# Kernel optimization log

Hardware: AMD Instinct MI355X
Metric: run time of the kernel (lower is better)

The kernel has to match this reference:

```python
import jax, jax.numpy as jnp
import numpy as np

N = 50000      # nodes
E = 1600000    # edges (avg degree 32)
IN, H, OUT, ED = 16, 128, 64, 16


def setup_inputs() -> dict:
    key = jax.random.key(0)
    ks = jax.random.split(key, 24)

    def w(k, shape):
        return jax.random.normal(k, shape, jnp.float32) / np.float32(np.sqrt(shape[0]))

    inp = {
        "x": jax.random.normal(ks[0], (N, IN), jnp.float32),
        "edge_attr": jax.random.normal(ks[1], (E, ED), jnp.float32),
        "edge_src": jax.random.randint(ks[2], (E,), 0, N, jnp.int32),
        "edge_dst": jax.random.randint(ks[3], (E,), 0, N, jnp.int32),
    }
    dims = [(IN, H, H), (H, H, H), (H, H, OUT)]
    i = 4
    for l, (din, dh, dout) in enumerate(dims):
        inp[f"we{l}"] = w(ks[i], (ED, din)); inp[f"be{l}"] = jnp.zeros((din,), jnp.float32)
        inp[f"w1{l}"] = w(ks[i + 1], (din, dh)); inp[f"b1{l}"] = jnp.zeros((dh,), jnp.float32)
        inp[f"w2{l}"] = w(ks[i + 2], (dh, dout)); inp[f"b2{l}"] = jnp.zeros((dout,), jnp.float32)
        i += 3
    inp["rw1"] = w(ks[i], (OUT, H)); inp["rb1"] = jnp.zeros((H,), jnp.float32)
    inp["rw2"] = w(ks[i + 1], (H, IN)); inp["rb2"] = jnp.zeros((IN,), jnp.float32)
    return inp


def reference(x, edge_attr, edge_src, edge_dst,
              we0, be0, w10, b10, w20, b20,
              we1, be1, w11, b11, w21, b21,
              we2, be2, w12, b12, w22, b22,
              rw1, rb1, rw2, rb2):
    layers = [(we0, be0, w10, b10, w20, b20),
              (we1, be1, w11, b11, w21, b21),
              (we2, be2, w12, b12, w22, b22)]
    n = x.shape[0]

    def phi(h):
        # GIN with edge features (GINE): h_i = MLP(h_i + sum_j relu(h_j + W_e e_ij))
        for idx, (we, be, w1, b1, w2, b2) in enumerate(layers):
            e = edge_attr @ we + be                                  # [E, d_in]
            msg = jax.nn.relu(h[edge_src] + e)                       # [E, d_in]
            agg = jax.ops.segment_sum(msg, edge_dst, num_segments=n)  # [N, d_in]
            h = jax.nn.relu((h + agg) @ w1 + b1) @ w2 + b2           # conv MLP
            if idx < len(layers) - 1:
                h = jax.nn.relu(h)
        return h

    out = phi(x) + phi(-x)                       # sign invariance, [N, OUT]
    out = jax.nn.relu(out @ rw1 + rb1) @ rw2 + rb2  # rho readout, [N, IN]
    return out
```

## Files before the change

kernel.cpp:

```cpp
#include <hip/hip_runtime.h>

constexpr int DHID = 128;

__device__ __forceinline__ float b2f(unsigned short u) {
    union { unsigned int i; float f; } v;
    v.i = ((unsigned int)u) << 16;
    return v.f;
}
__device__ __forceinline__ unsigned short f2b(float f) {
    union { float f; unsigned int i; } v;
    v.f = f;
    unsigned int x = v.i;
    return (unsigned short)((x + 0x7fff + ((x >> 16) & 1)) >> 16);
}
__device__ __forceinline__ unsigned int pack2(float a, float b) {
    return (unsigned int)f2b(a) | ((unsigned int)f2b(b) << 16);
}
__device__ __forceinline__ float bres(float w) { return w - b2f(f2b(w)); }
__device__ __forceinline__ void dot2b(float& acc, unsigned int a, unsigned int b) {
    asm("v_dot2_f32_bf16 %0, %1, %2, %0" : "+v"(acc) : "v"(a), "v"(b));
}

__global__ __launch_bounds__(256)
void init_h0(const float* __restrict__ x, float* __restrict__ H0,
             unsigned short* __restrict__ H0B, int n) {
    int i = blockIdx.x * 256 + threadIdx.x;
    if (i < n * 16) {
        int r = i >> 4, c = i & 15;
        float v = x[i];
        H0[(size_t)(2 * r) * 16 + c] = v;
        H0[(size_t)(2 * r + 1) * 16 + c] = -v;
        H0B[(size_t)(2 * r) * 16 + c] = f2b(v);
        H0B[(size_t)(2 * r + 1) * 16 + c] = f2b(-v);
    }
}

__global__ __launch_bounds__(256)
void sum_signs(const float* __restrict__ H3, float* __restrict__ S, int n) {
    int i = blockIdx.x * 256 + threadIdx.x;
    if (i < n * 64) {
        int r = i >> 6;
        S[i] = H3[i + (size_t)r * 64] + H3[i + (size_t)r * 64 + 64];
    }
}

__global__ __launch_bounds__(256)
void csr_count(const int* __restrict__ DST, int* __restrict__ deg, int E_) {
    int e = blockIdx.x * 256 + threadIdx.x;
    if (e < E_) atomicAdd(&deg[DST[e]], 1);
}

__global__ __launch_bounds__(256)
void scan1(const int* __restrict__ deg, int* __restrict__ off,
           int* __restrict__ bsum, int n) {
    __shared__ int s[256];
    int tid = threadIdx.x;
    int i = blockIdx.x * 256 + tid;
    int v = (i < n) ? deg[i] : 0;
    s[tid] = v;
    __syncthreads();
    for (int d = 1; d < 256; d <<= 1) {
        int t = (tid >= d) ? s[tid - d] : 0;
        __syncthreads();
        if (tid >= d) s[tid] += t;
        __syncthreads();
    }
    if (i < n) off[i] = s[tid] - v;
    if (tid == 255) bsum[blockIdx.x] = s[255];
}

__global__ __launch_bounds__(256)
void scan2(int* __restrict__ bsum, int nb) {
    __shared__ int s[256];
    int tid = threadIdx.x;
    int v = (tid < nb) ? bsum[tid] : 0;
    s[tid] = v;
    __syncthreads();
    for (int d = 1; d < 256; d <<= 1) {
        int t = (tid >= d) ? s[tid - d] : 0;
        __syncthreads();
        if (tid >= d) s[tid] += t;
        __syncthreads();
    }
    if (tid < nb) bsum[tid] = s[tid] - v;
}

__global__ __launch_bounds__(256)
void scan3(int* __restrict__ off, int* __restrict__ pos,
           const int* __restrict__ bsum, const int* __restrict__ deg, int n) {
    int i = blockIdx.x * 256 + threadIdx.x;
    if (i < n) {
        int o = off[i] + bsum[blockIdx.x];
        off[i] = o;
        pos[i] = o;
        if (i == n - 1) off[n] = o + deg[i];
    }
}

__global__ __launch_bounds__(256)
void csr_fill(const int* __restrict__ SRC, const int* __restrict__ DST,
              const float* __restrict__ EA, int* __restrict__ pos,
              int* __restrict__ csrsrc, uint4* __restrict__ EABS, int E_) {
    int e = blockIdx.x * 256 + threadIdx.x;
    if (e < E_) {
        int d = DST[e];
        int j = atomicAdd(&pos[d], 1);
        csrsrc[j] = SRC[e];
        const float4* ea4 = (const float4*)(EA + (size_t)e * 16);
        float4 q0 = ea4[0], q1 = ea4[1], q2 = ea4[2], q3 = ea4[3];
        uint4 o0, o1;
        o0.x = pack2(q0.x, q0.y); o0.y = pack2(q0.z, q0.w);
        o0.z = pack2(q1.x, q1.y); o0.w = pack2(q1.z, q1.w);
        o1.x = pack2(q2.x, q2.y); o1.y = pack2(q2.z, q2.w);
        o1.z = pack2(q3.x, q3.y); o1.w = pack2(q3.z, q3.w);
        EABS[(size_t)2 * j] = o0;
        EABS[(size_t)2 * j + 1] = o1;
    }
}

__global__ __launch_bounds__(256)
void agg_gather128(const int* __restrict__ CSRS, const int* __restrict__ OFF,
                   const uint4* __restrict__ EABS, const float* __restrict__ WE,
                   const float* __restrict__ BE,
                   const unsigned short* __restrict__ HB,
                   float* __restrict__ AGG, int n) {
    const int lane = threadIdx.x & 63;
    const int node = blockIdx.x * 4 + (threadIdx.x >> 6);
    if (node >= n) return;
    const int c = lane;
    unsigned int w0h[8], w0l[8], w1h[8], w1l[8];
#pragma unroll
    for (int t = 0; t < 8; ++t) {
        float a0 = WE[(2 * t) * 128 + c], a1 = WE[(2 * t + 1) * 128 + c];
        float b0 = WE[(2 * t) * 128 + c + 64], b1 = WE[(2 * t + 1) * 128 + c + 64];
        w0h[t] = pack2(a0, a1);
        w0l[t] = pack2(bres(a0), bres(a1));
        w1h[t] = pack2(b0, b1);
        w1l[t] = pack2(bres(b0), bres(b1));
    }
    const float be0 = BE[c], be1 = BE[c + 64];
    float a00 = 0.f, a01 = 0.f, a10 = 0.f, a11 = 0.f;
    const int j0 = OFF[node], j1 = OFF[node + 1];
#pragma unroll 4
    for (int j = j0; j < j1; ++j) {
        int src = CSRS[j];
        uint4 p = EABS[(size_t)2 * j], q = EABS[(size_t)2 * j + 1];
        float e0 = be0, e1 = be1;
        dot2b(e0, p.x, w0h[0]); dot2b(e0, p.y, w0h[1]);
        dot2b(e0, p.z, w0h[2]); dot2b(e0, p.w, w0h[3]);
        dot2b(e0, q.x, w0h[4]); dot2b(e0, q.y, w0h[5]);
        dot2b(e0, q.z, w0h[6]); dot2b(e0, q.w, w0h[7]);
        dot2b(e0, p.x, w0l[0]); dot2b(e0, p.y, w0l[1]);
        dot2b(e0, p.z, w0l[2]); dot2b(e0, p.w, w0l[3]);
        dot2b(e0, q.x, w0l[4]); dot2b(e0, q.y, w0l[5]);
        dot2b(e0, q.z, w0l[6]); dot2b(e0, q.w, w0l[7]);
        dot2b(e1, p.x, w1h[0]); dot2b(e1, p.y, w1h[1]);
        dot2b(e1, p.z, w1h[2]); dot2b(e1, p.w, w1h[3]);
        dot2b(e1, q.x, w1h[4]); dot2b(e1, q.y, w1h[5]);
        dot2b(e1, q.z, w1h[6]); dot2b(e1, q.w, w1h[7]);
        dot2b(e1, p.x, w1l[0]); dot2b(e1, p.y, w1l[1]);
        dot2b(e1, p.z, w1l[2]); dot2b(e1, p.w, w1l[3]);
        dot2b(e1, q.x, w1l[4]); dot2b(e1, q.y, w1l[5]);
        dot2b(e1, q.z, w1l[6]); dot2b(e1, q.w, w1l[7]);
        const unsigned short* h = HB + (size_t)(2 * src) * 128;
        a00 += fmaxf(b2f(h[c]) + e0, 0.f);
        a01 += fmaxf(b2f(h[c + 64]) + e1, 0.f);
        a10 += fmaxf(b2f(h[128 + c]) + e0, 0.f);
        a11 += fmaxf(b2f(h[128 + c + 64]) + e1, 0.f);
    }
    float* arow = AGG + (size_t)(2 * node) * 128;
    arow[c] = a00;
    arow[c + 64] = a01;
    arow[128 + c] = a10;
    arow[128 + c + 64] = a11;
}

__global__ __launch_bounds__(256)
void agg_gather16(const int* __restrict__ CSRS, const int* __restrict__ OFF,
                  const uint4* __restrict__ EABS, const float* __restrict__ WE,
                  const float* __restrict__ BE,
                  const unsigned short* __restrict__ HB,
                  float* __restrict__ AGG, int n) {
    const int l = threadIdx.x & 31;
    const int node = blockIdx.x * 8 + (threadIdx.x >> 5);
    if (node >= n) return;
    const int s = l >> 4;
    const int c = l & 15;
    unsigned int wh[8], wl[8];
#pragma unroll
    for (int t = 0; t < 8; ++t) {
        float a0 = WE[(2 * t) * 16 + c], a1 = WE[(2 * t + 1) * 16 + c];
        wh[t] = pack2(a0, a1);
        wl[t] = pack2(bres(a0), bres(a1));
    }
    const float bev = BE[c];
    float acc = 0.f;
    const int j0 = OFF[node], j1 = OFF[node + 1];
#pragma unroll 4
    for (int j = j0; j < j1; ++j) {
        int src = CSRS[j];
        uint4 p = EABS[(size_t)2 * j], q = EABS[(size_t)2 * j + 1];
        float ec = bev;
        dot2b(ec, p.x, wh[0]); dot2b(ec, p.y, wh[1]);
        dot2b(ec, p.z, wh[2]); dot2b(ec, p.w, wh[3]);
        dot2b(ec, q.x, wh[4]); dot2b(ec, q.y, wh[5]);
        dot2b(ec, q.z, wh[6]); dot2b(ec, q.w, wh[7]);
        dot2b(ec, p.x, wl[0]); dot2b(ec, p.y, wl[1]);
        dot2b(ec, p.z, wl[2]); dot2b(ec, p.w, wl[3]);
        dot2b(ec, q.x, wl[4]); dot2b(ec, q.y, wl[5]);
        dot2b(ec, q.z, wl[6]); dot2b(ec, q.w, wl[7]);
        float hv = b2f(HB[(size_t)(2 * src + s) * 16 + c]);
        acc += fmaxf(hv + ec, 0.f);
    }
    AGG[(size_t)(2 * node + s) * 16 + c] = acc;
}

template <int DIN, int DOUT, bool RELU_OUT, bool HAS_AGG, bool WRITE_B>
__global__ __launch_bounds__(256)
void node_mlp(const float* __restrict__ X, const float* __restrict__ AGG,
              const float* __restrict__ W1, const float* __restrict__ B1,
              const float* __restrict__ W2, const float* __restrict__ B2,
              float* __restrict__ OUT, unsigned short* __restrict__ OUTB,
              int rows) {
    __shared__ float sX[32 * DIN];
    __shared__ float sH[32 * DHID];
    const int tid = threadIdx.x;

    for (int row0 = blockIdx.x * 32; row0 < rows; row0 += gridDim.x * 32) {
        __syncthreads();
        constexpr int DIN4 = DIN / 4;
        for (int i = tid; i < 32 * DIN4; i += 256) {
            int r = i / DIN4, k4 = i % DIN4;
            int gr = row0 + r;
            float4 v = make_float4(0.f, 0.f, 0.f, 0.f);
            if (gr < rows) {
                v = ((const float4*)X)[(size_t)gr * DIN4 + k4];
                if (HAS_AGG) {
                    float4 a = ((const float4*)AGG)[(size_t)gr * DIN4 + k4];
                    v.x += a.x; v.y += a.y; v.z += a.z; v.w += a.w;
                }
            }
            ((float4*)sX)[i] = v;
        }
        __syncthreads();
        {
            const int c = tid & 63;
            const int r0 = tid >> 6;
            float acc[8][2];
            const float b1a = B1[c], b1b = B1[c + 64];
#pragma unroll
            for (int j = 0; j < 8; ++j) {
                acc[j][0] = b1a;
                acc[j][1] = b1b;
            }
#pragma unroll 2
            for (int k4 = 0; k4 < DIN / 4; ++k4) {
                const int k = 4 * k4;
                float wa[4], wb[4];
#pragma unroll
                for (int kk = 0; kk < 4; ++kk) {
                    wa[kk] = W1[(k + kk) * DHID + c];
                    wb[kk] = W1[(k + kk) * DHID + c + 64];
                }
#pragma unroll
                for (int j = 0; j < 8; ++j) {
                    float4 xv = ((const float4*)sX)[((r0 + 4 * j) * DIN + k) >> 2];
                    acc[j][0] += xv.x * wa[0]; acc[j][1] += xv.x * wb[0];
                    acc[j][0] += xv.y * wa[1]; acc[j][1] += xv.y * wb[1];
                    acc[j][0] += xv.z * wa[2]; acc[j][1] += xv.z * wb[2];
                    acc[j][0] += xv.w * wa[3]; acc[j][1] += xv.w * wb[3];
                }
            }
#pragma unroll
            for (int j = 0; j < 8; ++j) {
                int r = r0 + 4 * j;
                sH[r * DHID + c] = fmaxf(acc[j][0], 0.f);
                sH[r * DHID + c + 64] = fmaxf(acc[j][1], 0.f);
            }
        }
        __syncthreads();
        {
            constexpr int HALF = DOUT / 2;
            constexpr int RP = 256 / HALF;
            constexpr int ITER = 32 / RP;
            const int c = tid % HALF;
            const int r0 = tid / HALF;
            float acc[ITER][2];
            const float bz0 = B2[c], bz1 = B2[c + HALF];
#pragma unroll
            for (int j = 0; j < ITER; ++j) {
                acc[j][0] = bz0;
                acc[j][1] = bz1;
            }
#pragma unroll 2
            for (int k4 = 0; k4 < DHID / 4; ++k4) {
                const int k = 4 * k4;
                float wa[4], wb[4];
#pragma unroll
                for (int kk = 0; kk < 4; ++kk) {
                    wa[kk] = W2[(k + kk) * DOUT + c];
                    wb[kk] = W2[(k + kk) * DOUT + c + HALF];
                }
#pragma unroll
                for (int j = 0; j < ITER; ++j) {
                    float4 hv = ((const float4*)sH)[((r0 + RP * j) * DHID + k) >> 2];
                    acc[j][0] += hv.x * wa[0]; acc[j][1] += hv.x * wb[0];
                    acc[j][0] += hv.y * wa[1]; acc[j][1] += hv.y * wb[1];
                    acc[j][0] += hv.z * wa[2]; acc[j][1] += hv.z * wb[2];
                    acc[j][0] += hv.w * wa[3]; acc[j][1] += hv.w * wb[3];
                }
            }
#pragma unroll
            for (int j = 0; j < ITER; ++j) {
                int gr = row0 + r0 + RP * j;
                if (gr < rows) {
                    float o0 = acc[j][0], o1 = acc[j][1];
                    if (RELU_OUT) {
                        o0 = fmaxf(o0, 0.f);
                        o1 = fmaxf(o1, 0.f);
                    }
                    OUT[(size_t)gr * DOUT + c] = o0;
                    OUT[(size_t)gr * DOUT + c + HALF] = o1;
                    if (WRITE_B) {
                        OUTB[(size_t)gr * DOUT + c] = f2b(o0);
                        OUTB[(size_t)gr * DOUT + c + HALF] = f2b(o1);
                    }
                }
            }
        }
    }
}

extern "C" void kernel_launch(void* const* d_in, const int* in_sizes, int n_in,
                              void* d_out, int out_size, void* d_ws, size_t ws_size,
                              hipStream_t stream) {
    const float* x = (const float*)d_in[0];
    const float* ea = (const float*)d_in[1];
    const int* esrc = (const int*)d_in[2];
    const int* edst = (const int*)d_in[3];
    const float* we0 = (const float*)d_in[4];
    const float* be0 = (const float*)d_in[5];
    const float* w10 = (const float*)d_in[6];
    const float* b10 = (const float*)d_in[7];
    const float* w20 = (const float*)d_in[8];
    const float* b20 = (const float*)d_in[9];
    const float* we1 = (const float*)d_in[10];
    const float* be1 = (const float*)d_in[11];
    const float* w11 = (const float*)d_in[12];
    const float* b11 = (const float*)d_in[13];
    const float* w21 = (const float*)d_in[14];
    const float* b21 = (const float*)d_in[15];
    const float* we2 = (const float*)d_in[16];
    const float* be2 = (const float*)d_in[17];
    const float* w12 = (const float*)d_in[18];
    const float* b12 = (const float*)d_in[19];
    const float* w22 = (const float*)d_in[20];
    const float* b22 = (const float*)d_in[21];
    const float* rw1 = (const float*)d_in[22];
    const float* rb1 = (const float*)d_in[23];
    const float* rw2 = (const float*)d_in[24];
    const float* rb2 = (const float*)d_in[25];

    const int N = in_sizes[0] / 16;
    const int E = in_sizes[2];
    const int M = 2 * N;

    float* HA = (float*)d_ws;
    float* HB = HA + (size_t)M * 128;
    float* AG = HB + (size_t)M * 128;
    unsigned short* Hb = (unsigned short*)(AG + (size_t)M * 128);
    unsigned short* EABS = Hb + (size_t)M * 128;
    int* deg = (int*)(EABS + (size_t)E * 16);
    int* off = deg + N;
    int* pos = off + N + 1;
    int* bsum = pos + N;
    int* csrsrc = bsum + 256;

    const int ntiles = (M + 31) / 32;
    const int eblocks = (E + 255) / 256;
    const int nblocks = (N + 255) / 256;

    hipMemsetAsync(deg, 0, (size_t)N * sizeof(int), stream);
    csr_count<<<eblocks, 256, 0, stream>>>(edst, deg, E);
    scan1<<<nblocks, 256, 0, stream>>>(deg, off, bsum, N);
    scan2<<<1, 256, 0, stream>>>(bsum, nblocks);
    scan3<<<nblocks, 256, 0, stream>>>(off, pos, bsum, deg, N);
    csr_fill<<<eblocks, 256, 0, stream>>>(esrc, edst, ea, pos, csrsrc,
                                          (uint4*)EABS, E);

    init_h0<<<(N * 16 + 255) / 256, 256, 0, stream>>>(x, HA, Hb, N);

    agg_gather16<<<(N + 7) / 8, 256, 0, stream>>>(csrsrc, off, (const uint4*)EABS,
                                                  we0, be0, Hb, AG, N);
    node_mlp<16, 128, true, true, true><<<ntiles, 256, 0, stream>>>(
        HA, AG, w10, b10, w20, b20, HB, Hb, M);

    agg_gather128<<<(N + 3) / 4, 256, 0, stream>>>(csrsrc, off, (const uint4*)EABS,
                                                   we1, be1, Hb, AG, N);
    node_mlp<128, 128, true, true, true><<<ntiles, 256, 0, stream>>>(
        HB, AG, w11, b11, w21, b21, HA, Hb, M);

    agg_gather128<<<(N + 3) / 4, 256, 0, stream>>>(csrsrc, off, (const uint4*)EABS,
                                                   we2, be2, Hb, AG, N);
    node_mlp<128, 64, false, true, false><<<ntiles, 256, 0, stream>>>(
        HA, AG, w12, b12, w22, b22, HB, nullptr, M);

    sum_signs<<<(N * 64 + 255) / 256, 256, 0, stream>>>(HB, AG, N);
    node_mlp<64, 16, false, false, false><<<(N + 31) / 32, 256, 0, stream>>>(
        AG, nullptr, rw1, rb1, rw2, rb2, (float*)d_out, nullptr, N);
}
```

Before: 1.052 ms.

## Compute edge embeddings in 128-wide gather with MFMA bf16 tiles

Replaces the per-lane v_dot2 loop that computed the edge-feature projection in agg_gather128 with a 16x16x32 bf16 MFMA over 16 edges at a time. The hi/lo bf16 split of the weights is folded into the K dimension, so the two halves are summed inside one instruction. Each wave then handles 16 edges per iteration, gathers the source rows per output row, masks the tail, and reduces across lane groups with shuffles. This is meant to cut the VALU cost of the edge projection. In exchange it adds shuffle reductions, wasted MFMA work on partial tiles for low-degree nodes, and less coalesced gather loads.

```diff
diff --git a/kernel.cpp b/kernel.cpp
--- a/kernel.cpp
+++ b/kernel.cpp
@@ -1,6 +1,9 @@
 #include <hip/hip_runtime.h>
 
 constexpr int DHID = 128;
+
+typedef __attribute__((ext_vector_type(8))) short bf16x8v;
+typedef __attribute__((ext_vector_type(4))) float f32x4v;
 
 __device__ __forceinline__ float b2f(unsigned short u) {
     union { unsigned int i; float f; } v;
@@ -120,59 +123,92 @@
 
 __global__ __launch_bounds__(256)
 void agg_gather128(const int* __restrict__ CSRS, const int* __restrict__ OFF,
-                   const uint4* __restrict__ EABS, const float* __restrict__ WE,
-                   const float* __restrict__ BE,
+                   const unsigned short* __restrict__ EABS,
+                   const float* __restrict__ WE, const float* __restrict__ BE,
                    const unsigned short* __restrict__ HB,
                    float* __restrict__ AGG, int n) {
-    const int lane = threadIdx.x & 63;
-    const int node = blockIdx.x * 4 + (threadIdx.x >> 6);
+    const int tid = threadIdx.x;
+    const int lane = tid & 63;
+    const int node = blockIdx.x * 4 + (tid >> 6);
     if (node >= n) return;
-    const int c = lane;
-    unsigned int w0h[8], w0l[8], w1h[8], w1l[8];
-#pragma unroll
-    for (int t = 0; t < 8; ++t) {
-        float a0 = WE[(2 * t) * 128 + c], a1 = WE[(2 * t + 1) * 128 + c];
-        float b0 = WE[(2 * t) * 128 + c + 64], b1 = WE[(2 * t + 1) * 128 + c + 64];
-        w0h[t] = pack2(a0, a1);
-        w0l[t] = pack2(bres(a0), bres(a1));
-        w1h[t] = pack2(b0, b1);
-        w1l[t] = pack2(bres(b0), bres(b1));
-    }
-    const float be0 = BE[c], be1 = BE[c + 64];
-    float a00 = 0.f, a01 = 0.f, a10 = 0.f, a11 = 0.f;
+    const int col = lane & 15;
+    const int grp = lane >> 4;
+    const int klo = (grp & 1) * 8;
+
+    bf16x8v bfrag[8];
+#pragma unroll
+    for (int cb = 0; cb < 8; ++cb) {
+        bf16x8v b;
+#pragma unroll
+        for (int i = 0; i < 8; ++i) {
+            float w = WE[(klo + i) * 128 + cb * 16 + col];
+            unsigned short hi = f2b(w);
+            unsigned short lo = f2b(bres(w));
+            b[i] = (short)(grp >= 2 ? lo : hi);
+        }
+        bfrag[cb] = b;
+    }
+    float bias[8];
+#pragma unroll
+    for (int cb = 0; cb < 8; ++cb) bias[cb] = BE[cb * 16 + col];
+
+    float asum0[8], asum1[8];
+#pragma unroll
+    for (int cb = 0; cb < 8; ++cb) { asum0[cb] = 0.f; asum1[cb] = 0.f; }
+
     const int j0 = OFF[node], j1 = OFF[node + 1];
-#pragma unroll 4
-    for (int j = j0; j < j1; ++j) {
-        int src = CSRS[j];
-        uint4 p = EABS[(size_t)2 * j], q = EABS[(size_t)2 * j + 1];
-        float e0 = be0, e1 = be1;
-        dot2b(e0, p.x, w0h[0]); dot2b(e0, p.y, w0h[1]);
-        dot2b(e0, p.z, w0h[2]); dot2b(e0, p.w, w0h[3]);
-        dot2b(e0, q.x, w0h[4]); dot2b(e0, q.y, w0h[5]);
-        dot2b(e0, q.z, w0h[6]); dot2b(e0, q.w, w0h[7]);
-        dot2b(e0, p.x, w0l[0]); dot2b(e0, p.y, w0l[1]);
-        dot2b(e0, p.z, w0l[2]); dot2b(e0, p.w, w0l[3]);
-        dot2b(e0, q.x, w0l[4]); dot2b(e0, q.y, w0l[5]);
-        dot2b(e0, q.z, w0l[6]); dot2b(e0, q.w, w0l[7]);
-        dot2b(e1, p.x, w1h[0]); dot2b(e1, p.y, w1h[1]);
-        dot2b(e1, p.z, w1h[2]); dot2b(e1, p.w, w1h[3]);
-        dot2b(e1, q.x, w1h[4]); dot2b(e1, q.y, w1h[5]);
-        dot2b(e1, q.z, w1h[6]); dot2b(e1, q.w, w1h[7]);
-        dot2b(e1, p.x, w1l[0]); dot2b(e1, p.y, w1l[1]);
-        dot2b(e1, p.z, w1l[2]); dot2b(e1, p.w, w1l[3]);
-        dot2b(e1, q.x, w1l[4]); dot2b(e1, q.y, w1l[5]);
-        dot2b(e1, q.z, w1l[6]); dot2b(e1, q.w, w1l[7]);
-        const unsigned short* h = HB + (size_t)(2 * src) * 128;
-        a00 += fmaxf(b2f(h[c]) + e0, 0.f);
-        a01 += fmaxf(b2f(h[c + 64]) + e1, 0.f);
-        a10 += fmaxf(b2f(h[128 + c]) + e0, 0.f);
-        a11 += fmaxf(b2f(h[128 + c + 64]) + e1, 0.f);
+    const char* ebase = (const char*)EABS;
+
+    for (int base = j0; base < j1; base += 16) {
+        const int rem = j1 - base;
+        uint4 a4 = *(const uint4*)(ebase + ((size_t)(base + col) << 5) +
+                                   ((grp & 1) << 4));
+        bf16x8v afrag = __builtin_bit_cast(bf16x8v, a4);
+        f32x4v ev[8];
+#pragma unroll
+        for (int cb = 0; cb < 8; ++cb) {
+            f32x4v c = {bias[cb], bias[cb], bias[cb], bias[cb]};
+            ev[cb] = __builtin_amdgcn_mfma_f32_16x16x32_bf16(afrag, bfrag[cb], c,
+                                                             0, 0, 0);
+        }
+        float vmask[4];
+        const unsigned short* hp[4];
+#pragma unroll
+        for (int r = 0; r < 4; ++r) {
+            int t = grp * 4 + r;
+            bool valid = t < rem;
+            vmask[r] = valid ? 1.f : 0.f;
+            int ji = valid ? (base + t) : j0;
+            int src = CSRS[ji];
+            hp[r] = HB + (size_t)(2 * src) * 128;
+        }
+#pragma unroll
+        for (int cb = 0; cb < 8; ++cb) {
+            float p0 = 0.f, p1 = 0.f;
+#pragma unroll
+            for (int r = 0; r < 4; ++r) {
+                float e = ev[cb][r];
+                float h0 = b2f(hp[r][cb * 16 + col]);
+                float h1 = b2f(hp[r][128 + cb * 16 + col]);
+                p0 += fmaxf(h0 + e, 0.f) * vmask[r];
+                p1 += fmaxf(h1 + e, 0.f) * vmask[r];
+            }
+            p0 += __shfl_xor(p0, 16);
+            p0 += __shfl_xor(p0, 32);
+            p1 += __shfl_xor(p1, 16);
+            p1 += __shfl_xor(p1, 32);
+            asum0[cb] += p0;
+            asum1[cb] += p1;
+        }
     }
     float* arow = AGG + (size_t)(2 * node) * 128;
-    arow[c] = a00;
-    arow[c + 64] = a01;
-    arow[128 + c] = a10;
-    arow[128 + c + 64] = a11;
+#pragma unroll
+    for (int cb = 0; cb < 8; ++cb) {
+        if (grp == (cb & 3)) {
+            arow[cb * 16 + col] = asum0[cb];
+            arow[128 + cb * 16 + col] = asum1[cb];
+        }
+    }
 }
 
 __global__ __launch_bounds__(256)
@@ -395,12 +431,12 @@
     node_mlp<16, 128, true, true, true><<<ntiles, 256, 0, stream>>>(
         HA, AG, w10, b10, w20, b20, HB, Hb, M);
 
-    agg_gather128<<<(N + 3) / 4, 256, 0, stream>>>(csrsrc, off, (const uint4*)EABS,
+    agg_gather128<<<(N + 3) / 4, 256, 0, stream>>>(csrsrc, off, EABS,
                                                    we1, be1, Hb, AG, N);
     node_mlp<128, 128, true, true, true><<<ntiles, 256, 0, stream>>>(
         HB, AG, w11, b11, w21, b21, HA, Hb, M);
 
-    agg_gather128<<<(N + 3) / 4, 256, 0, stream>>>(csrsrc, off, (const uint4*)EABS,
+    agg_gather128<<<(N + 3) / 4, 256, 0, stream>>>(csrsrc, off, EABS,
                                                    we2, be2, Hb, AG, N);
     node_mlp<128, 64, false, true, false><<<ntiles, 256, 0, stream>>>(
         HA, AG, w12, b12, w22, b22, HB, nullptr, M);
```

Result: faster. 1.006 ms (-4.4%).
